# Performance work log

Hardware: AMD Instinct MI355X
Metric: run time of the kernel (lower is better)

## Reference

```python
import jax, jax.numpy as jnp
import numpy as np

H = 2048  # hidden_dim == input_dim


def _lstm_step(x, h, c, Wih, Whh, bih, bhh):
    # x: [1, in], h/c: [1, H]; PyTorch gate order: i, f, g, o along 4H axis
    gates = x @ Wih.T + h @ Whh.T + bih + bhh  # [1, 4H]
    i, f, g, o = jnp.split(gates, 4, axis=-1)
    c2 = jax.nn.sigmoid(f) * c + jax.nn.sigmoid(i) * jnp.tanh(g)
    h2 = jax.nn.sigmoid(o) * jnp.tanh(c2)
    return h2, c2


def setup_inputs() -> dict:
    key = jax.random.key(0)
    ks = jax.random.split(key, 20)
    s = 0.02
    inp = {
        "x": jax.random.normal(ks[0], (1,), dtype=jnp.float32),
        "input_hidden": jax.random.normal(ks[1], (3, 1, H), dtype=jnp.float32),
        "input_cell": jax.random.normal(ks[2], (3, 1, H), dtype=jnp.float32),
        # layer 0: input_size = 1
        "Wih0": jax.random.normal(ks[3], (4 * H, 1), dtype=jnp.float32) * s,
        "Whh0": jax.random.normal(ks[4], (4 * H, H), dtype=jnp.float32) * s,
        "bih0": jax.random.normal(ks[5], (4 * H,), dtype=jnp.float32) * s,
        "bhh0": jax.random.normal(ks[6], (4 * H,), dtype=jnp.float32) * s,
        # layers 1, 2: input_size = H
        "Wih1": jax.random.normal(ks[7], (4 * H, H), dtype=jnp.float32) * s,
        "Whh1": jax.random.normal(ks[8], (4 * H, H), dtype=jnp.float32) * s,
        "bih1": jax.random.normal(ks[9], (4 * H,), dtype=jnp.float32) * s,
        "bhh1": jax.random.normal(ks[10], (4 * H,), dtype=jnp.float32) * s,
        "Wih2": jax.random.normal(ks[11], (4 * H, H), dtype=jnp.float32) * s,
        "Whh2": jax.random.normal(ks[12], (4 * H, H), dtype=jnp.float32) * s,
        "bih2": jax.random.normal(ks[13], (4 * H,), dtype=jnp.float32) * s,
        "bhh2": jax.random.normal(ks[14], (4 * H,), dtype=jnp.float32) * s,
        # output projection: Linear(H, 1)
        "Wout": jax.random.normal(ks[15], (1, H), dtype=jnp.float32) * s,
        "bout": jax.random.normal(ks[16], (1,), dtype=jnp.float32) * s,
    }
    return inp


def reference(x, input_hidden, input_cell,
              Wih0, Whh0, bih0, bhh0,
              Wih1, Whh1, bih1, bhh1,
              Wih2, Whh2, bih2, bhh2,
              Wout, bout):
    # x.reshape((1,1,1)) in torch -> single timestep, batch 1, feature 1
    inp = x.reshape(1, 1)  # [batch=1, in=1]
    params = [(Wih0, Whh0, bih0, bhh0),
              (Wih1, Whh1, bih1, bhh1),
              (Wih2, Whh2, bih2, bhh2)]
    hs, cs = [], []
    layer_in = inp
    for l, (Wih, Whh, bih, bhh) in enumerate(params):  # fixed 3 layers
        h2, c2 = _lstm_step(layer_in, input_hidden[l], input_cell[l], Wih, Whh, bih, bhh)
        hs.append(h2)
        cs.append(c2)
        layer_in = h2
    hidden_n = jnp.stack(hs, axis=0)  # [3, 1, H]
    cell_n = jnp.stack(cs, axis=0)    # [3, 1, H]
    # top-layer output [1,1,H] -> Linear -> [1,1,1]
    y = (layer_in @ Wout.T + bout).reshape(1, 1, 1)
    return y, hidden_n, cell_n
```

## Files before the change

kernel.cpp:

```cpp
#include <hip/hip_runtime.h>
#include <math.h>

#define H 2048

__device__ __forceinline__ float sigmoidf_(float v) {
    return 1.0f / (1.0f + expf(-v));
}

__device__ __forceinline__ float wave_reduce_sum(float v) {
    v += __shfl_down(v, 32, 64);
    v += __shfl_down(v, 16, 64);
    v += __shfl_down(v, 8, 64);
    v += __shfl_down(v, 4, 64);
    v += __shfl_down(v, 2, 64);
    v += __shfl_down(v, 1, 64);
    return v;
}

__device__ __forceinline__ float row_dot(const float4* __restrict__ Wr,
                                         const float4* __restrict__ v4,
                                         int lane) {
    float4 a[8];
#pragma unroll
    for (int k = 0; k < 8; ++k) a[k] = Wr[lane + 64 * k];
    float acc = 0.0f;
#pragma unroll
    for (int k = 0; k < 8; ++k) {
        float4 b = v4[lane + 64 * k];
        acc += a[k].x * b.x + a[k].y * b.y + a[k].z * b.z + a[k].w * b.w;
    }
    return acc;
}

__global__ __launch_bounds__(256)
void lstm_layer0(const float* __restrict__ Wih0,
                 const float* __restrict__ Whh,
                 const float* __restrict__ bih,
                 const float* __restrict__ bhh,
                 const float* __restrict__ xs,
                 const float* __restrict__ hin,
                 const float* __restrict__ cin,
                 float* __restrict__ hout,
                 float* __restrict__ cout)
{
    __shared__ float hv[H];
    __shared__ float dots[4];
    const int t = blockIdx.x;
    const int tid = threadIdx.x;

    {
        const float4* h4 = (const float4*)hin;
        float4* hs = (float4*)hv;
        hs[tid] = h4[tid];
        hs[tid + 256] = h4[tid + 256];
    }
    __syncthreads();

    const int w = tid >> 6;
    const int lane = tid & 63;
    const size_t row = (size_t)w * H + t;

    float acc = row_dot((const float4*)(Whh + row * H), (const float4*)hv, lane);
    acc = wave_reduce_sum(acc);
    if (lane == 0) dots[w] = acc;
    __syncthreads();

    if (tid == 0) {
        const float x = xs[0];
        float gi = dots[0] + x * Wih0[t]         + bih[t]         + bhh[t];
        float gf = dots[1] + x * Wih0[H + t]     + bih[H + t]     + bhh[H + t];
        float gg = dots[2] + x * Wih0[2 * H + t] + bih[2 * H + t] + bhh[2 * H + t];
        float go = dots[3] + x * Wih0[3 * H + t] + bih[3 * H + t] + bhh[3 * H + t];
        float c2 = sigmoidf_(gf) * cin[t] + sigmoidf_(gi) * tanhf(gg);
        float h2 = sigmoidf_(go) * tanhf(c2);
        cout[t] = c2;
        hout[t] = h2;
    }
}

__global__ __launch_bounds__(512)
void lstm_layer_mat(const float* __restrict__ Wih,
                    const float* __restrict__ Whh,
                    const float* __restrict__ bih,
                    const float* __restrict__ bhh,
                    const float* __restrict__ xin,
                    const float* __restrict__ hin,
                    const float* __restrict__ cin,
                    float* __restrict__ hout,
                    float* __restrict__ cout)
{
    __shared__ float xv[H];
    __shared__ float hv[H];
    __shared__ float dots[8];
    const int t = blockIdx.x;
    const int tid = threadIdx.x;

    {
        const float4* x4 = (const float4*)xin;
        const float4* h4 = (const float4*)hin;
        ((float4*)xv)[tid] = x4[tid];
        ((float4*)hv)[tid] = h4[tid];
    }
    __syncthreads();

    const int w = tid >> 6;
    const int lane = tid & 63;
    const int gate = w & 3;
    const float* W = (w < 4) ? Wih : Whh;
    const float* v = (w < 4) ? xv : hv;
    const size_t row = (size_t)gate * H + t;

    float acc = row_dot((const float4*)(W + row * H), (const float4*)v, lane);
    acc = wave_reduce_sum(acc);
    if (lane == 0) dots[w] = acc;
    __syncthreads();

    if (tid == 0) {
        float gi = dots[0] + dots[4] + bih[t]         + bhh[t];
        float gf = dots[1] + dots[5] + bih[H + t]     + bhh[H + t];
        float gg = dots[2] + dots[6] + bih[2 * H + t] + bhh[2 * H + t];
        float go = dots[3] + dots[7] + bih[3 * H + t] + bhh[3 * H + t];
        float c2 = sigmoidf_(gf) * cin[t] + sigmoidf_(gi) * tanhf(gg);
        float h2 = sigmoidf_(go) * tanhf(c2);
        cout[t] = c2;
        hout[t] = h2;
    }
}

__global__ __launch_bounds__(256)
void out_proj(const float* __restrict__ Wout,
              const float* __restrict__ bout,
              const float* __restrict__ h,
              float* __restrict__ y)
{
    __shared__ float part[4];
    const int tid = threadIdx.x;
    const float4* W4 = (const float4*)Wout;
    const float4* h4 = (const float4*)h;
    float acc = 0.0f;
#pragma unroll
    for (int k = 0; k < 2; ++k) {
        int i = tid + 256 * k;
        float4 a = W4[i];
        float4 b = h4[i];
        acc += a.x * b.x + a.y * b.y + a.z * b.z + a.w * b.w;
    }
    acc = wave_reduce_sum(acc);
    if ((tid & 63) == 0) part[tid >> 6] = acc;
    __syncthreads();
    if (tid == 0) y[0] = part[0] + part[1] + part[2] + part[3] + bout[0];
}

extern "C" void kernel_launch(void* const* d_in, const int* in_sizes, int n_in,
                              void* d_out, int out_size, void* d_ws, size_t ws_size,
                              hipStream_t stream) {
    const float* x    = (const float*)d_in[0];
    const float* hin  = (const float*)d_in[1];
    const float* cin  = (const float*)d_in[2];
    const float* Wih0 = (const float*)d_in[3];
    const float* Whh0 = (const float*)d_in[4];
    const float* bih0 = (const float*)d_in[5];
    const float* bhh0 = (const float*)d_in[6];
    const float* Wih1 = (const float*)d_in[7];
    const float* Whh1 = (const float*)d_in[8];
    const float* bih1 = (const float*)d_in[9];
    const float* bhh1 = (const float*)d_in[10];
    const float* Wih2 = (const float*)d_in[11];
    const float* Whh2 = (const float*)d_in[12];
    const float* bih2 = (const float*)d_in[13];
    const float* bhh2 = (const float*)d_in[14];
    const float* Wout = (const float*)d_in[15];
    const float* bout = (const float*)d_in[16];

    float* out = (float*)d_out;
    float* y  = out;
    float* hN = out + 1;
    float* cN = out + 1 + 3 * H;

    lstm_layer0<<<H, 256, 0, stream>>>(Wih0, Whh0, bih0, bhh0, x,
                                       hin, cin, hN, cN);
    lstm_layer_mat<<<H, 512, 0, stream>>>(Wih1, Whh1, bih1, bhh1,
                                          hN, hin + H, cin + H,
                                          hN + H, cN + H);
    lstm_layer_mat<<<H, 512, 0, stream>>>(Wih2, Whh2, bih2, bhh2,
                                          hN + H, hin + 2 * H, cin + 2 * H,
                                          hN + 2 * H, cN + 2 * H);
    out_proj<<<1, 256, 0, stream>>>(Wout, bout, hN + 2 * H, y);
}
```

Before: 326.9 us.

## Assign one wave per hidden unit with register-held input vectors

Each wavefront now computes all four gate rows for one hidden unit, looping over the gates, so there is no longer one block per hidden unit with shared-memory staging and two block barriers. The input and hidden vectors are loaded once into registers per wave, and each block handles four hidden units. This removes the LDS traffic and barriers but gives each wave serialized gate loops with fewer independent loads in flight, and it raises register pressure from holding 16 float4 vectors.

```diff
diff --git a/kernel.cpp b/kernel.cpp
--- a/kernel.cpp
+++ b/kernel.cpp
@@ -17,60 +17,47 @@
     return v;
 }
 
-__device__ __forceinline__ float row_dot(const float4* __restrict__ Wr,
-                                         const float4* __restrict__ v4,
-                                         int lane) {
-    float4 a[8];
-#pragma unroll
-    for (int k = 0; k < 8; ++k) a[k] = Wr[lane + 64 * k];
-    float acc = 0.0f;
+__global__ __launch_bounds__(256, 2)
+void lstm_layer(const float* __restrict__ Wih, const float* __restrict__ Whh,
+                const float* __restrict__ bih, const float* __restrict__ bhh,
+                const float* __restrict__ xin,
+                const float* __restrict__ hin,
+                const float* __restrict__ cin,
+                float* __restrict__ hout, float* __restrict__ cout)
+{
+    const int t = blockIdx.x * 4 + (threadIdx.x >> 6);
+    const int lane = threadIdx.x & 63;
+
+    float4 xv[8], hv[8];
+    const float4* x4 = (const float4*)xin;
+    const float4* h4 = (const float4*)hin;
 #pragma unroll
     for (int k = 0; k < 8; ++k) {
-        float4 b = v4[lane + 64 * k];
-        acc += a[k].x * b.x + a[k].y * b.y + a[k].z * b.z + a[k].w * b.w;
+        xv[k] = x4[lane + 64 * k];
+        hv[k] = h4[lane + 64 * k];
     }
-    return acc;
-}
 
-__global__ __launch_bounds__(256)
-void lstm_layer0(const float* __restrict__ Wih0,
-                 const float* __restrict__ Whh,
-                 const float* __restrict__ bih,
-                 const float* __restrict__ bhh,
-                 const float* __restrict__ xs,
-                 const float* __restrict__ hin,
-                 const float* __restrict__ cin,
-                 float* __restrict__ hout,
-                 float* __restrict__ cout)
-{
-    __shared__ float hv[H];
-    __shared__ float dots[4];
-    const int t = blockIdx.x;
-    const int tid = threadIdx.x;
+    float gsum[4];
+#pragma unroll 1
+    for (int g = 0; g < 4; ++g) {
+        const float4* wi = (const float4*)(Wih + (size_t)(g * H + t) * H);
+        const float4* wh = (const float4*)(Whh + (size_t)(g * H + t) * H);
+        float ai = 0.0f, ah = 0.0f;
+#pragma unroll
+        for (int k = 0; k < 8; ++k) {
+            float4 a = wi[lane + 64 * k];
+            float4 b = wh[lane + 64 * k];
+            ai += a.x * xv[k].x + a.y * xv[k].y + a.z * xv[k].z + a.w * xv[k].w;
+            ah += b.x * hv[k].x + b.y * hv[k].y + b.z * hv[k].z + b.w * hv[k].w;
+        }
+        gsum[g] = wave_reduce_sum(ai + ah);
+    }
 
-    {
-        const float4* h4 = (const float4*)hin;
-        float4* hs = (float4*)hv;
-        hs[tid] = h4[tid];
-        hs[tid + 256] = h4[tid + 256];
-    }
-    __syncthreads();
-
-    const int w = tid >> 6;
-    const int lane = tid & 63;
-    const size_t row = (size_t)w * H + t;
-
-    float acc = row_dot((const float4*)(Whh + row * H), (const float4*)hv, lane);
-    acc = wave_reduce_sum(acc);
-    if (lane == 0) dots[w] = acc;
-    __syncthreads();
-
-    if (tid == 0) {
-        const float x = xs[0];
-        float gi = dots[0] + x * Wih0[t]         + bih[t]         + bhh[t];
-        float gf = dots[1] + x * Wih0[H + t]     + bih[H + t]     + bhh[H + t];
-        float gg = dots[2] + x * Wih0[2 * H + t] + bih[2 * H + t] + bhh[2 * H + t];
-        float go = dots[3] + x * Wih0[3 * H + t] + bih[3 * H + t] + bhh[3 * H + t];
+    if (lane == 0) {
+        float gi = gsum[0] + bih[t]         + bhh[t];
+        float gf = gsum[1] + bih[H + t]     + bhh[H + t];
+        float gg = gsum[2] + bih[2 * H + t] + bhh[2 * H + t];
+        float go = gsum[3] + bih[3 * H + t] + bhh[3 * H + t];
         float c2 = sigmoidf_(gf) * cin[t] + sigmoidf_(gi) * tanhf(gg);
         float h2 = sigmoidf_(go) * tanhf(c2);
         cout[t] = c2;
@@ -78,48 +65,43 @@
     }
 }
 
-__global__ __launch_bounds__(512)
-void lstm_layer_mat(const float* __restrict__ Wih,
-                    const float* __restrict__ Whh,
-                    const float* __restrict__ bih,
-                    const float* __restrict__ bhh,
-                    const float* __restrict__ xin,
-                    const float* __restrict__ hin,
-                    const float* __restrict__ cin,
-                    float* __restrict__ hout,
-                    float* __restrict__ cout)
+__global__ __launch_bounds__(256, 2)
+void lstm_layer0(const float* __restrict__ Wih0,
+                 const float* __restrict__ Whh,
+                 const float* __restrict__ bih, const float* __restrict__ bhh,
+                 const float* __restrict__ xs,
+                 const float* __restrict__ hin, const float* __restrict__ cin,
+                 float* __restrict__ hout, float* __restrict__ cout)
 {
-    __shared__ float xv[H];
-    __shared__ float hv[H];
-    __shared__ float dots[8];
-    const int t = blockIdx.x;
-    const int tid = threadIdx.x;
+    const int t = blockIdx.x * 4 + (threadIdx.x >> 6);
+    const int lane = threadIdx.x & 63;
 
-    {
-        const float4* x4 = (const float4*)xin;
-        const float4* h4 = (const float4*)hin;
-        ((float4*)xv)[tid] = x4[tid];
-        ((float4*)hv)[tid] = h4[tid];
+    float4 hv[8];
+    const float4* h4 = (const float4*)hin;
+#pragma unroll
+    for (int k = 0; k < 8; ++k) hv[k] = h4[lane + 64 * k];
+
+    float gsum[4];
+#pragma unroll 1
+    for (int g = 0; g < 4; ++g) {
+        const float4* wh = (const float4*)(Whh + (size_t)(g * H + t) * H);
+        float a0 = 0.0f, a1 = 0.0f;
+#pragma unroll
+        for (int k = 0; k < 8; k += 2) {
+            float4 a = wh[lane + 64 * k];
+            float4 b = wh[lane + 64 * (k + 1)];
+            a0 += a.x * hv[k].x + a.y * hv[k].y + a.z * hv[k].z + a.w * hv[k].w;
+            a1 += b.x * hv[k+1].x + b.y * hv[k+1].y + b.z * hv[k+1].z + b.w * hv[k+1].w;
+        }
+        gsum[g] = wave_reduce_sum(a0 + a1);
     }
-    __syncthreads();
 
-    const int w = tid >> 6;
-    const int lane = tid & 63;
-    const int gate = w & 3;
-    const float* W = (w < 4) ? Wih : Whh;
-    const float* v = (w < 4) ? xv : hv;
-    const size_t row = (size_t)gate * H + t;
-
-    float acc = row_dot((const float4*)(W + row * H), (const float4*)v, lane);
-    acc = wave_reduce_sum(acc);
-    if (lane == 0) dots[w] = acc;
-    __syncthreads();
-
-    if (tid == 0) {
-        float gi = dots[0] + dots[4] + bih[t]         + bhh[t];
-        float gf = dots[1] + dots[5] + bih[H + t]     + bhh[H + t];
-        float gg = dots[2] + dots[6] + bih[2 * H + t] + bhh[2 * H + t];
-        float go = dots[3] + dots[7] + bih[3 * H + t] + bhh[3 * H + t];
+    if (lane == 0) {
+        const float x = xs[0];
+        float gi = gsum[0] + x * Wih0[t]         + bih[t]         + bhh[t];
+        float gf = gsum[1] + x * Wih0[H + t]     + bih[H + t]     + bhh[H + t];
+        float gg = gsum[2] + x * Wih0[2 * H + t] + bih[2 * H + t] + bhh[2 * H + t];
+        float go = gsum[3] + x * Wih0[3 * H + t] + bih[3 * H + t] + bhh[3 * H + t];
         float c2 = sigmoidf_(gf) * cin[t] + sigmoidf_(gi) * tanhf(gg);
         float h2 = sigmoidf_(go) * tanhf(c2);
         cout[t] = c2;
@@ -133,7 +115,7 @@
               const float* __restrict__ h,
               float* __restrict__ y)
 {
-    __shared__ float part[4];
+    __shared__ float partl[4];
     const int tid = threadIdx.x;
     const float4* W4 = (const float4*)Wout;
     const float4* h4 = (const float4*)h;
@@ -146,9 +128,9 @@
         acc += a.x * b.x + a.y * b.y + a.z * b.z + a.w * b.w;
     }
     acc = wave_reduce_sum(acc);
-    if ((tid & 63) == 0) part[tid >> 6] = acc;
+    if ((tid & 63) == 0) partl[tid >> 6] = acc;
     __syncthreads();
-    if (tid == 0) y[0] = part[0] + part[1] + part[2] + part[3] + bout[0];
+    if (tid == 0) y[0] = partl[0] + partl[1] + partl[2] + partl[3] + bout[0];
 }
 
 extern "C" void kernel_launch(void* const* d_in, const int* in_sizes, int n_in,
@@ -177,13 +159,13 @@
     float* hN = out + 1;
     float* cN = out + 1 + 3 * H;
 
-    lstm_layer0<<<H, 256, 0, stream>>>(Wih0, Whh0, bih0, bhh0, x,
-                                       hin, cin, hN, cN);
-    lstm_layer_mat<<<H, 512, 0, stream>>>(Wih1, Whh1, bih1, bhh1,
-                                          hN, hin + H, cin + H,
-                                          hN + H, cN + H);
-    lstm_layer_mat<<<H, 512, 0, stream>>>(Wih2, Whh2, bih2, bhh2,
-                                          hN + H, hin + 2 * H, cin + 2 * H,
-                                          hN + 2 * H, cN + 2 * H);
+    lstm_layer0<<<512, 256, 0, stream>>>(Wih0, Whh0, bih0, bhh0, x,
+                                         hin, cin, hN, cN);
+    lstm_layer<<<512, 256, 0, stream>>>(Wih1, Whh1, bih1, bhh1,
+                                        hN, hin + H, cin + H,
+                                        hN + H, cN + H);
+    lstm_layer<<<512, 256, 0, stream>>>(Wih2, Whh2, bih2, bhh2,
+                                        hN + H, hin + 2 * H, cin + 2 * H,
+                                        hN + 2 * H, cN + 2 * H);
     out_proj<<<1, 256, 0, stream>>>(Wout, bout, hN + 2 * H, y);
 }
```

Measured after the change: 319.3 us. 1.02x faster.
